# Performance work log

Hardware: AMD Instinct MI355X
Metric: run time of the kernel (lower is better)

Reference implementation:

```python
import jax, jax.numpy as jnp
import numpy as np
import math

B, L, H, E, D = 4, 2048, 8, 64, 64


def _build_local_log_symmetry_mask(L):
    # Faithful port of LocalLogSymmetryMask: True = masked-out position.
    lws = math.ceil(np.log2(L) / 2)  # local window size
    n_log = math.ceil(10 * np.log2(L))
    m = np.zeros((L, L), dtype=np.float32)
    for i in range(L):
        row = m[i]
        # left side: local window + log-spaced long-range
        if i - lws + 1 < 0:
            row[:i] = 1
        else:
            row[i - lws + 1:i + 1] = 1
            for k in range(n_log):
                ni = i - lws + 1 - int(1.5 ** k)
                if ni >= 0:
                    row[ni] = 1
                else:
                    break
        # right side (symmetric)
        if i + lws - 1 >= L:
            row[i:] = 1
        else:
            row[i:i + lws] = 1
            for k in range(n_log):
                ni = i + lws - 1 + int(1.5 ** k)
                if ni < L:
                    row[ni] = 1
                else:
                    break
    return m == 0  # True where attention is NOT allowed


def setup_inputs() -> dict:
    key = jax.random.key(0)
    kq, kk, kv = jax.random.split(key, 3)
    queries = jax.random.normal(kq, (B, L, H, E), dtype=jnp.float32)
    keys = jax.random.normal(kk, (B, L, H, E), dtype=jnp.float32)
    values = jax.random.normal(kv, (B, L, H, D), dtype=jnp.float32)
    mask = jnp.asarray(_build_local_log_symmetry_mask(L))  # [L, L] bool
    return {"queries": queries, "keys": keys, "values": values, "mask": mask}


def reference(queries, keys, values, mask):
    # queries/keys: [B,L,H,E], values: [B,L,H,D], mask: [L,L] bool (True = masked)
    E_ = queries.shape[-1]
    scale = 1.0 / math.sqrt(E_)
    # scores: [B,H,L,S]
    scores = jnp.einsum("blhe,bshe->bhls", queries, keys) * scale
    scores = jnp.where(mask[None, None, :, :], -jnp.inf, scores)
    attn = jax.nn.softmax(scores, axis=-1)  # dropout disabled (eval mode)
    out = jnp.einsum("bhls,bshd->blhd", attn, values)  # [B,L,H,D]
    return out
```

## Files before the change

kernel.cpp:

```cpp
#include <hip/hip_runtime.h>


#define KB 4
#define KL 2048
#define KH 8
#define KE 64
#define KWAVES 4
#define KROWS (KB * KL * KH)
#define KBLOCKS (KROWS / KWAVES)
#define KROWB (KH * KE * 4)

static constexpr int kOff[48] = {
    -5, -4, -3, -2, -1, 0, 1, 2, 3, 4, 5,
    -6, -7, -8, -10, -12, -16, -22, -30, -43, -62, -91, -134, -199, -296,
    -442, -661, -990, -1482,
    6, 7, 8, 10, 12, 16, 22, 30, 43, 62, 91, 134, 199, 296, 442, 661, 990,
    1482,
    1 << 19};

template <int CTRL>
__device__ __forceinline__ float dpp_radd(float x) {
    int t = __builtin_amdgcn_update_dpp(0, __float_as_int(x), CTRL, 0xF, 0xF,
                                        false);
    return x + __int_as_float(t);
}

#if __has_builtin(__builtin_amdgcn_permlane16_swap)
__device__ __forceinline__ void pl16(float x, float& a, float& b) {
    auto r = __builtin_amdgcn_permlane16_swap(__float_as_uint(x),
                                              __float_as_uint(x), false, false);
    a = __uint_as_float(r[0]);
    b = __uint_as_float(r[1]);
}
#else
__device__ __forceinline__ void pl16(float x, float& a, float& b) {
    a = x;
    b = __shfl_xor(x, 16, 64);
}
#endif

#if __has_builtin(__builtin_amdgcn_permlane32_swap)
__device__ __forceinline__ void pl32(float x, float& a, float& b) {
    auto r = __builtin_amdgcn_permlane32_swap(__float_as_uint(x),
                                              __float_as_uint(x), false, false);
    a = __uint_as_float(r[0]);
    b = __uint_as_float(r[1]);
}
#else
__device__ __forceinline__ void pl32(float x, float& a, float& b) {
    a = x;
    b = __shfl_xor(x, 32, 64);
}
#endif

__device__ __forceinline__ float red16_add(float x) {
    float a, b;
    pl16(x, a, b);
    return a + b;
}
__device__ __forceinline__ float red32_add(float x) {
    float a, b;
    pl32(x, a, b);
    return a + b;
}

#if __has_builtin(__builtin_amdgcn_exp2f)
#define KEXP2(x) __builtin_amdgcn_exp2f(x)
#else
#define KEXP2(x) exp2f(x)
#endif

__global__ __launch_bounds__(256, 6) void MaskAttention_20572893347881_kernel(
    const float* __restrict__ q, const float* __restrict__ k,
    const float* __restrict__ v, float* __restrict__ out) {
    const int tid  = (int)threadIdx.x;
    const int lane = tid & 63;
    const int g    = lane >> 4;
    const int e4   = lane & 15;
    const int wave = __builtin_amdgcn_readfirstlane(tid >> 6);

    const int p = (int)blockIdx.x;
    const int l = (p & 7) * (KBLOCKS / 8) + (p >> 3);
    const int r = l * KWAVES + wave;
    const int i = r & (KL - 1);
    const int h = (r >> 11) & (KH - 1);
    const int b = r >> 14;

    const unsigned hbB = (unsigned)b * (unsigned)(KL * KROWB) +
                         (unsigned)h * (unsigned)(KE * 4);
    const char* __restrict__ qc = (const char*)q + hbB;
    const char* __restrict__ kc = (const char*)k + hbB;
    const char* __restrict__ vc = (const char*)v + hbB;
    char* __restrict__ oc       = (char*)out + hbB;

    const unsigned co     = (unsigned)(e4 * 16);
    const unsigned base   = (unsigned)i * (unsigned)KROWB + co;
    const unsigned clampv = (unsigned)((KL - 1) * KROWB) + co;

    const bool g1 = (g & 1) != 0;
    const bool g2 = (g & 2) != 0;

    unsigned off[12];
    bool ok[12];
#pragma unroll
    for (int t = 0; t < 12; ++t) {
        const int a0 = kOff[4 * t + 0] * KROWB;
        const int a1 = kOff[4 * t + 1] * KROWB;
        const int a2 = kOff[4 * t + 2] * KROWB;
        const int a3 = kOff[4 * t + 3] * KROWB;
        const int dd = g1 ? (g2 ? a3 : a1) : (g2 ? a2 : a0);
        const unsigned u = base + (unsigned)dd;
        ok[t]  = u < (unsigned)(KL * KROWB);
        off[t] = u < clampv ? u : clampv;
    }

    float4 qf = *(const float4*)(qc + base);
    const float qs = 0.125f * 1.44269504088896340736f;
    qf.x *= qs;
    qf.y *= qs;
    qf.z *= qs;
    qf.w *= qs;

    float d0s = 0.f, d1s = 0.f;
    float4 acc0 = make_float4(0.f, 0.f, 0.f, 0.f);
    float4 acc1 = make_float4(0.f, 0.f, 0.f, 0.f);
#pragma unroll
    for (int t = 0; t < 12; ++t) {
        const float4 kf = *(const float4*)(kc + off[t]);
        const float4 vf = *(const float4*)(vc + off[t]);
        float sd = qf.x * kf.x + qf.y * kf.y + qf.z * kf.z + qf.w * kf.w;
        sd = dpp_radd<0x121>(sd);
        sd = dpp_radd<0x122>(sd);
        sd = dpp_radd<0x124>(sd);
        sd = dpp_radd<0x128>(sd);
        const float pr = ok[t] ? KEXP2(sd) : 0.f;
        if (t & 1) {
            d1s += pr;
            acc1.x += pr * vf.x;
            acc1.y += pr * vf.y;
            acc1.z += pr * vf.z;
            acc1.w += pr * vf.w;
        } else {
            d0s += pr;
            acc0.x += pr * vf.x;
            acc0.y += pr * vf.y;
            acc0.z += pr * vf.z;
            acc0.w += pr * vf.w;
        }
    }

    float d = d0s + d1s;
    d = red16_add(d);
    d = red32_add(d);
    const float inv = __builtin_amdgcn_rcpf(d);

    float4 acc = make_float4(acc0.x + acc1.x, acc0.y + acc1.y,
                             acc0.z + acc1.z, acc0.w + acc1.w);
    acc.x = red16_add(acc.x);
    acc.y = red16_add(acc.y);
    acc.z = red16_add(acc.z);
    acc.w = red16_add(acc.w);
    acc.x = red32_add(acc.x);
    acc.y = red32_add(acc.y);
    acc.z = red32_add(acc.z);
    acc.w = red32_add(acc.w);

    if (lane < 16) {
        float4 o = make_float4(acc.x * inv, acc.y * inv, acc.z * inv,
                               acc.w * inv);
        *(float4*)(oc + base) = o;
    }
}

extern "C" void kernel_launch(void* const* d_in, const int* in_sizes, int n_in,
                              void* d_out, int out_size, void* d_ws,
                              size_t ws_size, hipStream_t stream) {
    (void)in_sizes; (void)n_in; (void)out_size; (void)d_ws; (void)ws_size;
    const float* q = (const float*)d_in[0];
    const float* k = (const float*)d_in[1];
    const float* v = (const float*)d_in[2];
    float* out = (float*)d_out;

    hipLaunchKernelGGL(MaskAttention_20572893347881_kernel, dim3(KBLOCKS),
                       dim3(KWAVES * 64), 0, stream, q, k, v, out);
}
```

Measured before the change: 150.4 us.

## Pre-pack K and V into an interleaved fp16 workspace for the sparse attention kernel

Adds a prep kernel that converts K and V to fp16 and interleaves them into one 256-byte row per (b,h,position), stored in the workspace. The main kernel then does a single 16-byte load per gathered key instead of two fp32 loads, and computes dot products with fdot2, using DPP moves to share q halves and p across lanes. The aim is to halve the bytes gathered in the sparse pass and cut the load count. The cost is an extra launch plus a full read of K and V and a write of the packed copy, along with fp16 rounding of K, V and Q. A fp32 fallback path is kept for when no workspace is available.

```diff
diff --git a/kernel.cpp b/kernel.cpp
--- a/kernel.cpp
+++ b/kernel.cpp
@@ -9,6 +9,11 @@
 #define KROWS (KB * KL * KH)
 #define KBLOCKS (KROWS / KWAVES)
 #define KROWB (KH * KE * 4)
+#define KVROWB 256
+#define KWSBYTES ((size_t)KROWS * KVROWB)
+
+typedef __fp16 h2 __attribute__((ext_vector_type(2)));
+typedef unsigned ui4 __attribute__((ext_vector_type(4)));
 
 static constexpr int kOff[48] = {
     -5, -4, -3, -2, -1, 0, 1, 2, 3, 4, 5,
@@ -24,6 +29,11 @@
                                         false);
     return x + __int_as_float(t);
 }
+template <int CTRL>
+__device__ __forceinline__ unsigned dpp_mov_u(unsigned x) {
+    return (unsigned)__builtin_amdgcn_update_dpp(0, (int)x, CTRL, 0xF, 0xF,
+                                                 false);
+}
 
 #if __has_builtin(__builtin_amdgcn_permlane16_swap)
 __device__ __forceinline__ void pl16(float x, float& a, float& b) {
@@ -38,7 +48,6 @@
     b = __shfl_xor(x, 16, 64);
 }
 #endif
-
 #if __has_builtin(__builtin_amdgcn_permlane32_swap)
 __device__ __forceinline__ void pl32(float x, float& a, float& b) {
     auto r = __builtin_amdgcn_permlane32_swap(__float_as_uint(x),
@@ -52,7 +61,6 @@
     b = __shfl_xor(x, 32, 64);
 }
 #endif
-
 __device__ __forceinline__ float red16_add(float x) {
     float a, b;
     pl16(x, a, b);
@@ -70,7 +78,153 @@
 #define KEXP2(x) exp2f(x)
 #endif
 
-__global__ __launch_bounds__(256, 6) void MaskAttention_20572893347881_kernel(
+__device__ __forceinline__ h2 pkrtz(float a, float b) {
+#if __has_builtin(__builtin_amdgcn_cvt_pkrtz)
+    return __builtin_amdgcn_cvt_pkrtz(a, b);
+#else
+    h2 r;
+    r[0] = (__fp16)a;
+    r[1] = (__fp16)b;
+    return r;
+#endif
+}
+__device__ __forceinline__ float fd2(h2 a, h2 b, float c) {
+#if __has_builtin(__builtin_amdgcn_fdot2)
+    return __builtin_amdgcn_fdot2(a, b, c, false);
+#else
+    return fmaf((float)a[1], (float)b[1], fmaf((float)a[0], (float)b[0], c));
+#endif
+}
+__device__ __forceinline__ h2 as_h2(unsigned u) {
+    return __builtin_bit_cast(h2, u);
+}
+
+__global__ __launch_bounds__(256) void MaskAttention_prep_kernel(
+    const float* __restrict__ k, const float* __restrict__ v,
+    unsigned* __restrict__ kv) {
+    const unsigned t  = (unsigned)blockIdx.x * 256u + (unsigned)threadIdx.x;
+    const unsigned qd = t & 15u;
+    const unsigned gr = t >> 4;
+    const unsigned j  = gr & (KL - 1);
+    const unsigned bh = gr >> 11;
+    const unsigned b  = bh >> 3;
+    const unsigned h  = bh & 7;
+    const unsigned m  = qd >> 1;
+    const float* __restrict__ src = (qd & 1u) ? v : k;
+    const float* s =
+        src + ((((size_t)b * KL + j) * KH + h) * KE + (size_t)m * 8);
+    const float4 x = *(const float4*)s;
+    const float4 y = *(const float4*)(s + 4);
+    ui4 o;
+    o[0] = __builtin_bit_cast(unsigned, pkrtz(x.x, x.y));
+    o[1] = __builtin_bit_cast(unsigned, pkrtz(x.z, x.w));
+    o[2] = __builtin_bit_cast(unsigned, pkrtz(y.x, y.y));
+    o[3] = __builtin_bit_cast(unsigned, pkrtz(y.z, y.w));
+    *(ui4*)((char*)kv + (size_t)gr * KVROWB + (size_t)qd * 16) = o;
+}
+
+__global__ __launch_bounds__(256) void MaskAttention_20572893347881_kernel(
+    const float* __restrict__ q, const unsigned* __restrict__ kv,
+    float* __restrict__ out) {
+    const int tid  = (int)threadIdx.x;
+    const int lane = tid & 63;
+    const int g    = lane >> 4;
+    const int e4   = lane & 15;
+    const int wave = __builtin_amdgcn_readfirstlane(tid >> 6);
+
+    const int p = (int)blockIdx.x;
+    const int l = (p & 7) * (KBLOCKS / 8) + (p >> 3);
+    const int r = l * KWAVES + wave;
+    const int i  = r & (KL - 1);
+    const int bh = r >> 11;
+
+    const char* __restrict__ kvb =
+        (const char*)kv + (size_t)bh * (KL * KVROWB);
+    const size_t hbB = (size_t)(bh >> 3) * (KL * KROWB) +
+                       (size_t)(bh & 7) * (KE * 4);
+    const char* __restrict__ qc = (const char*)q + hbB;
+    char* __restrict__ oc       = (char*)out + hbB;
+
+    const unsigned co     = (unsigned)(e4 * 16);
+    const unsigned base_r = (unsigned)i * KVROWB + co;
+    const unsigned clampv = (unsigned)(KL - 1) * KVROWB + co;
+
+    const bool g1 = (g & 1) != 0;
+    const bool g2 = (g & 2) != 0;
+
+    unsigned off[12];
+    bool ok[12];
+#pragma unroll
+    for (int t = 0; t < 12; ++t) {
+        const int a0 = kOff[4 * t + 0] * KVROWB;
+        const int a1 = kOff[4 * t + 1] * KVROWB;
+        const int a2 = kOff[4 * t + 2] * KVROWB;
+        const int a3 = kOff[4 * t + 3] * KVROWB;
+        const int dd = g1 ? (g2 ? a3 : a1) : (g2 ? a2 : a0);
+        const unsigned u = base_r + (unsigned)dd;
+        ok[t]  = u < (unsigned)(KL * KVROWB);
+        off[t] = u < clampv ? u : clampv;
+    }
+
+    const float4 qf = *(const float4*)(qc + (unsigned)i * KROWB + co);
+    const float qs  = 0.125f * 1.44269504088896340736f;
+    const h2 qa = pkrtz(qf.x * qs, qf.y * qs);
+    const h2 qb = pkrtz(qf.z * qs, qf.w * qs);
+    const h2 qan =
+        as_h2(dpp_mov_u<0x101>(__builtin_bit_cast(unsigned, qa)));
+    const h2 qbn =
+        as_h2(dpp_mov_u<0x101>(__builtin_bit_cast(unsigned, qb)));
+
+    float dsum = 0.f;
+    float a0 = 0.f, a1 = 0.f, a2 = 0.f, a3 = 0.f;
+    float a4 = 0.f, a5 = 0.f, a6 = 0.f, a7 = 0.f;
+#pragma unroll
+    for (int t = 0; t < 12; ++t) {
+        const ui4 w = *(const ui4*)(kvb + off[t]);
+        float sd = fd2(as_h2(w[0]), qa,
+                       fd2(as_h2(w[1]), qb,
+                           fd2(as_h2(w[2]), qan, fd2(as_h2(w[3]), qbn, 0.f))));
+        sd = dpp_radd<0x122>(sd);
+        sd = dpp_radd<0x124>(sd);
+        sd = dpp_radd<0x128>(sd);
+        const float pp = ok[t] ? KEXP2(sd) : 0.f;
+        const float pv =
+            __uint_as_float(dpp_mov_u<0x111>(__float_as_uint(pp)));
+        dsum += pv;
+        const h2 v01 = as_h2(w[0]), v23 = as_h2(w[1]);
+        const h2 v45 = as_h2(w[2]), v67 = as_h2(w[3]);
+        a0 = fmaf(pv, (float)v01[0], a0);
+        a1 = fmaf(pv, (float)v01[1], a1);
+        a2 = fmaf(pv, (float)v23[0], a2);
+        a3 = fmaf(pv, (float)v23[1], a3);
+        a4 = fmaf(pv, (float)v45[0], a4);
+        a5 = fmaf(pv, (float)v45[1], a5);
+        a6 = fmaf(pv, (float)v67[0], a6);
+        a7 = fmaf(pv, (float)v67[1], a7);
+    }
+
+    float d = red32_add(red16_add(dsum));
+    const float inv = __builtin_amdgcn_rcpf(d);
+    a0 = red32_add(red16_add(a0));
+    a1 = red32_add(red16_add(a1));
+    a2 = red32_add(red16_add(a2));
+    a3 = red32_add(red16_add(a3));
+    a4 = red32_add(red16_add(a4));
+    a5 = red32_add(red16_add(a5));
+    a6 = red32_add(red16_add(a6));
+    a7 = red32_add(red16_add(a7));
+
+    if ((lane < 16) && (lane & 1)) {
+        const int m = lane >> 1;
+        char* dst = oc + (unsigned)i * KROWB + (unsigned)m * 32;
+        float4 o0 = make_float4(a0 * inv, a1 * inv, a2 * inv, a3 * inv);
+        float4 o1 = make_float4(a4 * inv, a5 * inv, a6 * inv, a7 * inv);
+        *(float4*)dst = o0;
+        *(float4*)(dst + 16) = o1;
+    }
+}
+
+__global__ __launch_bounds__(256) void MaskAttention_f32_fallback_kernel(
     const float* __restrict__ q, const float* __restrict__ k,
     const float* __restrict__ v, float* __restrict__ out) {
     const int tid  = (int)threadIdx.x;
@@ -78,28 +232,22 @@
     const int g    = lane >> 4;
     const int e4   = lane & 15;
     const int wave = __builtin_amdgcn_readfirstlane(tid >> 6);
-
     const int p = (int)blockIdx.x;
     const int l = (p & 7) * (KBLOCKS / 8) + (p >> 3);
     const int r = l * KWAVES + wave;
     const int i = r & (KL - 1);
     const int h = (r >> 11) & (KH - 1);
     const int b = r >> 14;
-
-    const unsigned hbB = (unsigned)b * (unsigned)(KL * KROWB) +
-                         (unsigned)h * (unsigned)(KE * 4);
+    const size_t hbB = (size_t)b * (KL * KROWB) + (size_t)h * (KE * 4);
     const char* __restrict__ qc = (const char*)q + hbB;
     const char* __restrict__ kc = (const char*)k + hbB;
     const char* __restrict__ vc = (const char*)v + hbB;
     char* __restrict__ oc       = (char*)out + hbB;
-
     const unsigned co     = (unsigned)(e4 * 16);
-    const unsigned base   = (unsigned)i * (unsigned)KROWB + co;
+    const unsigned base   = (unsigned)i * KROWB + co;
     const unsigned clampv = (unsigned)((KL - 1) * KROWB) + co;
-
     const bool g1 = (g & 1) != 0;
     const bool g2 = (g & 2) != 0;
-
     unsigned off[12];
     bool ok[12];
 #pragma unroll
@@ -113,17 +261,11 @@
         ok[t]  = u < (unsigned)(KL * KROWB);
         off[t] = u < clampv ? u : clampv;
     }
-
     float4 qf = *(const float4*)(qc + base);
     const float qs = 0.125f * 1.44269504088896340736f;
-    qf.x *= qs;
-    qf.y *= qs;
-    qf.z *= qs;
-    qf.w *= qs;
-
-    float d0s = 0.f, d1s = 0.f;
-    float4 acc0 = make_float4(0.f, 0.f, 0.f, 0.f);
-    float4 acc1 = make_float4(0.f, 0.f, 0.f, 0.f);
+    qf.x *= qs; qf.y *= qs; qf.z *= qs; qf.w *= qs;
+    float dsum = 0.f;
+    float4 acc = make_float4(0.f, 0.f, 0.f, 0.f);
 #pragma unroll
     for (int t = 0; t < 12; ++t) {
         const float4 kf = *(const float4*)(kc + off[t]);
@@ -134,37 +276,18 @@
         sd = dpp_radd<0x124>(sd);
         sd = dpp_radd<0x128>(sd);
         const float pr = ok[t] ? KEXP2(sd) : 0.f;
-        if (t & 1) {
-            d1s += pr;
-            acc1.x += pr * vf.x;
-            acc1.y += pr * vf.y;
-            acc1.z += pr * vf.z;
-            acc1.w += pr * vf.w;
-        } else {
-            d0s += pr;
-            acc0.x += pr * vf.x;
-            acc0.y += pr * vf.y;
-            acc0.z += pr * vf.z;
-            acc0.w += pr * vf.w;
-        }
-    }
-
-    float d = d0s + d1s;
-    d = red16_add(d);
-    d = red32_add(d);
+        dsum += pr;
+        acc.x = fmaf(pr, vf.x, acc.x);
+        acc.y = fmaf(pr, vf.y, acc.y);
+        acc.z = fmaf(pr, vf.z, acc.z);
+        acc.w = fmaf(pr, vf.w, acc.w);
+    }
+    float d = red32_add(red16_add(dsum));
     const float inv = __builtin_amdgcn_rcpf(d);
-
-    float4 acc = make_float4(acc0.x + acc1.x, acc0.y + acc1.y,
-                             acc0.z + acc1.z, acc0.w + acc1.w);
-    acc.x = red16_add(acc.x);
-    acc.y = red16_add(acc.y);
-    acc.z = red16_add(acc.z);
-    acc.w = red16_add(acc.w);
-    acc.x = red32_add(acc.x);
-    acc.y = red32_add(acc.y);
-    acc.z = red32_add(acc.z);
-    acc.w = red32_add(acc.w);
-
+    acc.x = red32_add(red16_add(acc.x));
+    acc.y = red32_add(red16_add(acc.y));
+    acc.z = red32_add(red16_add(acc.z));
+    acc.w = red32_add(red16_add(acc.w));
     if (lane < 16) {
         float4 o = make_float4(acc.x * inv, acc.y * inv, acc.z * inv,
                                acc.w * inv);
@@ -175,12 +298,23 @@
 extern "C" void kernel_launch(void* const* d_in, const int* in_sizes, int n_in,
                               void* d_out, int out_size, void* d_ws,
                               size_t ws_size, hipStream_t stream) {
-    (void)in_sizes; (void)n_in; (void)out_size; (void)d_ws; (void)ws_size;
+    (void)in_sizes; (void)n_in; (void)out_size;
     const float* q = (const float*)d_in[0];
     const float* k = (const float*)d_in[1];
     const float* v = (const float*)d_in[2];
     float* out = (float*)d_out;
 
-    hipLaunchKernelGGL(MaskAttention_20572893347881_kernel, dim3(KBLOCKS),
-                       dim3(KWAVES * 64), 0, stream, q, k, v, out);
-}
+    if (d_ws != nullptr && ws_size >= KWSBYTES) {
+        unsigned* kv = (unsigned*)d_ws;
+        hipLaunchKernelGGL(MaskAttention_prep_kernel,
+                           dim3(KROWS * 16 / 256), dim3(256), 0, stream,
+                           k, v, kv);
+        hipLaunchKernelGGL(MaskAttention_20572893347881_kernel,
+                           dim3(KBLOCKS), dim3(KWAVES * 64), 0, stream,
+                           q, kv, out);
+    } else {
+        hipLaunchKernelGGL(MaskAttention_f32_fallback_kernel,
+                           dim3(KBLOCKS), dim3(KWAVES * 64), 0, stream,
+                           q, k, v, out);
+    }
+}
```

Result: faster. 142.9 us (-5.0%).
